# Kernel optimization log

Hardware: AMD Instinct MI355X
Metric: run time of the kernel (lower is better)

The kernel has to match this reference:

```python
import jax, jax.numpy as jnp
import numpy as np

B, N = 2, 256
RC = 6.0
BOX = 12.0
# (center_radius, eta) for G2; kappas for G3; (eta, zeta, lambda) for G4/G5
G2_PARAMS = [(rs, eta) for rs in (0.0, 2.0) for eta in (0.1, 1.0)]
G3_KAPPAS = [1.0, 2.0]
G45_PARAMS = [(eta, zeta, lam) for eta in (0.01, 0.1) for zeta in (1.0, 4.0) for lam in (-1.0, 1.0)]


def _fc(r, rc):
    # Behler cosine cutoff: 0.5*(cos(pi r / rc) + 1) for r < rc, else 0
    return 0.5 * (jnp.cos(jnp.pi * r / rc) + 1.0) * (r < rc)


def setup_inputs() -> dict:
    key = jax.random.key(0)
    k1, k2 = jax.random.split(key)
    atomic_numbers = jax.random.randint(k1, (N,), 1, 10).astype(jnp.float32)
    coordinates = jax.random.uniform(k2, (B, N, 3), dtype=jnp.float32) * BOX
    return {"atomic_numbers": atomic_numbers, "coordinates": coordinates}


def reference(atomic_numbers, coordinates):
    b, n, _ = coordinates.shape
    # r_ij vector = x_i - x_j, matching coords.unsqueeze(-2) - coords.unsqueeze(-3)
    dvec = coordinates[:, :, None, :] - coordinates[:, None, :, :]        # [B,N,N,3]
    sq = jnp.sum(dvec * dvec, axis=-1)                                    # [B,N,N]
    pair_mask = ~jnp.eye(n, dtype=bool)                                   # j != i
    sq_safe = jnp.where(pair_mask, sq, 1.0)
    r = jnp.where(pair_mask, jnp.sqrt(sq_safe), 0.0)                      # [B,N,N]
    fcr = _fc(r, RC) * pair_mask                                          # cutoff, self excluded

    feats = [jnp.broadcast_to(atomic_numbers, (b, n))]
    # G1: sum_j fc(r_ij)
    feats.append(jnp.sum(fcr, axis=-1))
    # G2: sum_j exp(-eta*(r_ij - Rs)^2) * fc(r_ij)
    for rs, eta in G2_PARAMS:
        feats.append(jnp.sum(jnp.exp(-eta * (r - rs) ** 2) * fcr, axis=-1))
    # G3: sum_j cos(kappa * r_ij) * fc(r_ij)
    for kappa in G3_KAPPAS:
        feats.append(jnp.sum(jnp.cos(kappa * r) * fcr, axis=-1))

    # shared angular (triplet) quantities, each [B,N,N,N]
    dot = jnp.einsum('bijc,bikc->bijk', dvec, dvec)
    denom = r[:, :, :, None] * r[:, :, None, :]
    cos_t = dot / jnp.where(denom > 0, denom, 1.0)
    sq_ij = sq[:, :, :, None]
    sq_ik = sq[:, :, None, :]
    sq_jk = sq[:, None, :, :]
    sq3 = sq_ij + sq_ik + sq_jk
    sq2 = sq_ij + sq_ik
    # fc products: fcr already zero on the diagonal, so fc3 vanishes whenever
    # j==i, k==i, or j==k (full triplet mask for G4)
    fc3 = fcr[:, :, :, None] * fcr[:, :, None, :] * fcr[:, None, :, :]
    fc2 = fcr[:, :, :, None] * fcr[:, :, None, :] * pair_mask[None, None, :, :]

    # G4: 2^(1-zeta) sum_{j!=k} (1+lam*cos)^zeta exp(-eta*(rij^2+rik^2+rjk^2)) fc fc fc
    for eta, zeta, lam in G45_PARAMS:
        ang = jnp.maximum(1.0 + lam * cos_t, 0.0) ** zeta
        feats.append((2.0 ** (1.0 - zeta)) * jnp.sum(ang * jnp.exp(-eta * sq3) * fc3, axis=(-2, -1)))
    # G5: 2^(1-zeta) sum_{j!=k} (1+lam*cos)^zeta exp(-eta*(rij^2+rik^2)) fc fc
    for eta, zeta, lam in G45_PARAMS:
        ang = jnp.maximum(1.0 + lam * cos_t, 0.0) ** zeta
        feats.append((2.0 ** (1.0 - zeta)) * jnp.sum(ang * jnp.exp(-eta * sq2) * fc2, axis=(-2, -1)))

    return jnp.stack(feats, axis=-1)  # [B, N, 24]
```

## Files before the change

### kernel.cpp

```cpp
#include <hip/hip_runtime.h>
#include <math.h>

#define NN 256
#define NF 24
#define RCUT 6.0f
#define PI_F 3.14159265358979323846f
#define NSEG 8

__global__ __launch_bounds__(512, 4) void feat_kernel(
    const float* __restrict__ Z,
    const float* __restrict__ coords,
    float* __restrict__ out)
{
    const int i = blockIdx.x, b = blockIdx.y;
    const int tid = threadIdx.x, lane = tid & 63, wave = tid >> 6;

    __shared__ float4 geo[NN];
    __shared__ float2 ab[NN];
    __shared__ int   wave_cnt[4];
    __shared__ float rad[4][7];
    __shared__ float red2[8][8][16];

    const float* cb = coords + (size_t)b * NN * 3;
    const float xi = cb[i * 3 + 0], yi = cb[i * 3 + 1], zi = cb[i * 3 + 2];

    float dx = 0, dy = 0, dz = 0, r2 = 0, r = 0, fc = 0;
    bool incut = false;
    if (tid < NN) {
        const float xj = cb[tid * 3 + 0], yj = cb[tid * 3 + 1], zj = cb[tid * 3 + 2];
        dx = xi - xj; dy = yi - yj; dz = zi - zj;
        r2 = dx * dx + dy * dy + dz * dz;
        r  = sqrtf(r2);
        incut = (tid != i) && (r < RCUT);
        fc = incut ? 0.5f * (__cosf((PI_F / RCUT) * r) + 1.0f) : 0.0f;

        float racc[7];
        racc[0] = fc;
        racc[1] = __expf(-0.1f * r2) * fc;
        racc[2] = __expf(-1.0f * r2) * fc;
        const float d = r - 2.0f;
        racc[3] = __expf(-0.1f * d * d) * fc;
        racc[4] = __expf(-1.0f * d * d) * fc;
        racc[5] = __cosf(r) * fc;
        racc[6] = __cosf(2.0f * r) * fc;
#pragma unroll
        for (int t = 0; t < 7; t++) {
            float v = racc[t];
            for (int off = 32; off > 0; off >>= 1) v += __shfl_down(v, off, 64);
            if (lane == 0) rad[wave][t] = v;
        }
        const unsigned long long bal = __ballot(incut);
        if (lane == 0) wave_cnt[wave] = __popcll(bal);
    }
    __syncthreads();

    const int m = wave_cnt[0] + wave_cnt[1] + wave_cnt[2] + wave_cnt[3];
    if (tid < NN && incut) {
        const unsigned long long bal = __ballot(incut);
        int base = 0;
#pragma unroll
        for (int w = 0; w < 4; w++) if (w < wave) base += wave_cnt[w];
        const int p = base + __popcll(bal & ((1ULL << lane) - 1ULL));
        geo[p] = make_float4(dx, dy, dz, 1.0f / r);
        ab[p]  = make_float2(fc * __expf(-0.01f * r2), fc * __expf(-0.1f * r2));
    }
    __syncthreads();

    float acc[16];
#pragma unroll
    for (int t = 0; t < 16; t++) acc[t] = 0.0f;

    if (m >= 2) {
        const int Rfull = (m - 1) >> 1;
        const int tlo = 1 + (Rfull * wave) / NSEG;
        const int thi = (Rfull * (wave + 1)) / NSEG;
        const bool halfseg = (wave == NSEG - 1) && ((m & 1) == 0);
        const int mh = m >> 1;
        for (int rnd = 0; rnd < 4; ++rnd) {
            const int jj = lane + (rnd << 6);
            if (jj >= m) break;
            const float4 gj = geo[jj];
            const float2 aj = ab[jj];
            const int tend = thi + ((halfseg && jj < mh) ? 1 : 0);
#pragma unroll 2
            for (int t = tlo; t <= tend; ++t) {
                int kk = jj + ((t > thi) ? mh : t); if (kk >= m) kk -= m;
                const float4 g = geo[kk];
                const float2 a = ab[kk];
                const float ddx = gj.x - g.x, ddy = gj.y - g.y, ddz = gj.z - g.z;
                const float sqjk = ddx * ddx + ddy * ddy + ddz * ddz;
                const float rjk = sqrtf(sqjk);
                const float fcjk = (rjk < RCUT) ? 0.5f * (__cosf((PI_F / RCUT) * rjk) + 1.0f) : 0.0f;
                const float dot = gj.x * g.x + gj.y * g.y + gj.z * g.z;
                const float cost = dot * gj.w * g.w;
                const float w2a = aj.x * a.x;
                const float w2b = aj.y * a.y;
                const float t3a = fcjk * __expf(-0.01f * sqjk);
                const float t3b = fcjk * __expf(-0.1f * sqjk);
                const float w3a = w2a * t3a, w3b = w2b * t3b;
                const float c1m = 1.0f - cost;
                const float c1p = 1.0f + cost;
                const float c2m = c1m * c1m, c2p = c1p * c1p;
                const float c4m = c2m * c2m, c4p = c2p * c2p;
                acc[0]  += c1m * w3a;  acc[1]  += c1p * w3a;
                acc[2]  += c4m * w3a;  acc[3]  += c4p * w3a;
                acc[4]  += c1m * w3b;  acc[5]  += c1p * w3b;
                acc[6]  += c4m * w3b;  acc[7]  += c4p * w3b;
                acc[8]  += c1m * w2a;  acc[9]  += c1p * w2a;
                acc[10] += c4m * w2a;  acc[11] += c4p * w2a;
                acc[12] += c1m * w2b;  acc[13] += c1p * w2b;
                acc[14] += c4m * w2b;  acc[15] += c4p * w2b;
            }
        }
    }

#pragma unroll
    for (int t = 0; t < 16; t++) {
        float v = acc[t];
        v += __shfl_down(v, 32, 64);
        v += __shfl_down(v, 16, 64);
        v += __shfl_down(v, 8, 64);
        acc[t] = v;
    }
    if (lane < 8) {
#pragma unroll
        for (int t = 0; t < 16; t++) red2[wave][lane][t] = acc[t];
    }
    __syncthreads();

    float* ob = out + ((size_t)b * NN + i) * NF;
    if (tid < 128) {
        const int f = tid >> 3, s = tid & 7;
        float v = 0.0f;
#pragma unroll
        for (int w = 0; w < 8; w++) v += red2[w][s][f];
        v += __shfl_down(v, 4, 8);
        v += __shfl_down(v, 2, 8);
        v += __shfl_down(v, 1, 8);
        if (s == 0) {
            v *= ((f & 3) >= 2) ? 0.25f : 2.0f;
            ob[8 + f] = v;
        }
    } else if (tid >= 128 && tid < 135) {
        const int t = tid - 128;
        ob[1 + t] = rad[0][t] + rad[1][t] + rad[2][t] + rad[3][t];
    } else if (tid == 135) {
        ob[0] = Z[i];
    }
}

extern "C" void kernel_launch(void* const* d_in, const int* in_sizes, int n_in,
                              void* d_out, int out_size, void* d_ws, size_t ws_size,
                              hipStream_t stream) {
    const float* Z = (const float*)d_in[0];
    const float* coords = (const float*)d_in[1];
    float* out = (float*)d_out;
    feat_kernel<<<dim3(NN, 2), dim3(512), 0, stream>>>(Z, coords, out);
}
```

Baseline: 65.86 us.

## Split G4 and G5 triplet sums across separate blocks, replicate neighbor list

Launches a third grid dimension so that one block per atom computes the G4 (three-cutoff) accumulators and another computes the G5 (two-cutoff) ones, halving per-thread accumulators. The neighbor arrays are extended with a wrapped copy so the inner loop indexes kk = jj + t directly, with no modulo branch. The G5 half skips the sqrt, cos and exp work on r_jk. In exchange the neighbor-list construction is duplicated across both blocks, the block count doubles, and the two halves carry unequal work.

Result: no change. 65.52 us (-0.5%).

```diff
diff --git a/kernel.cpp b/kernel.cpp
--- a/kernel.cpp
+++ b/kernel.cpp
@@ -7,19 +7,84 @@
 #define PI_F 3.14159265358979323846f
 #define NSEG 8
 
+template <bool TRIPLE>
+__device__ __forceinline__ void pair_loop(
+    const float4* __restrict__ geo, const float2* __restrict__ ab,
+    int m, int wave, int lane, float* acc)
+{
+    const int Rfull = (m - 1) >> 1;
+    const int tlo = 1 + ((Rfull * wave) >> 3);
+    const int thi = (Rfull * (wave + 1)) >> 3;
+    const int mh = m >> 1;
+    for (int rnd = 0; rnd < 4; ++rnd) {
+        const int jj = lane + (rnd << 6);
+        if (jj >= m) break;
+        const float4 gj = geo[jj];
+        const float2 aj = ab[jj];
+        for (int t = tlo; t <= thi; ++t) {
+            const int kk = jj + t;
+            const float4 g = geo[kk];
+            const float2 a = ab[kk];
+            const float dot = gj.x * g.x + gj.y * g.y + gj.z * g.z;
+            const float cost = dot * gj.w * g.w;
+            float wa = aj.x * a.x;
+            float wb = aj.y * a.y;
+            if (TRIPLE) {
+                const float ddx = gj.x - g.x, ddy = gj.y - g.y, ddz = gj.z - g.z;
+                const float sqjk = ddx * ddx + ddy * ddy + ddz * ddz;
+                const float rjk = sqrtf(sqjk);
+                const float fcjk = (rjk < RCUT) ? 0.5f * (__cosf((PI_F / RCUT) * rjk) + 1.0f) : 0.0f;
+                wa *= fcjk * __expf(-0.01f * sqjk);
+                wb *= fcjk * __expf(-0.1f * sqjk);
+            }
+            const float c1m = 1.0f - cost, c1p = 1.0f + cost;
+            const float c2m = c1m * c1m, c2p = c1p * c1p;
+            const float c4m = c2m * c2m, c4p = c2p * c2p;
+            acc[0] += c1m * wa;  acc[1] += c1p * wa;
+            acc[2] += c4m * wa;  acc[3] += c4p * wa;
+            acc[4] += c1m * wb;  acc[5] += c1p * wb;
+            acc[6] += c4m * wb;  acc[7] += c4p * wb;
+        }
+        if (wave == NSEG - 1 && (m & 1) == 0 && jj < mh) {
+            const int kk = jj + mh;
+            const float4 g = geo[kk];
+            const float2 a = ab[kk];
+            const float dot = gj.x * g.x + gj.y * g.y + gj.z * g.z;
+            const float cost = dot * gj.w * g.w;
+            float wa = aj.x * a.x;
+            float wb = aj.y * a.y;
+            if (TRIPLE) {
+                const float ddx = gj.x - g.x, ddy = gj.y - g.y, ddz = gj.z - g.z;
+                const float sqjk = ddx * ddx + ddy * ddy + ddz * ddz;
+                const float rjk = sqrtf(sqjk);
+                const float fcjk = (rjk < RCUT) ? 0.5f * (__cosf((PI_F / RCUT) * rjk) + 1.0f) : 0.0f;
+                wa *= fcjk * __expf(-0.01f * sqjk);
+                wb *= fcjk * __expf(-0.1f * sqjk);
+            }
+            const float c1m = 1.0f - cost, c1p = 1.0f + cost;
+            const float c2m = c1m * c1m, c2p = c1p * c1p;
+            const float c4m = c2m * c2m, c4p = c2p * c2p;
+            acc[0] += c1m * wa;  acc[1] += c1p * wa;
+            acc[2] += c4m * wa;  acc[3] += c4p * wa;
+            acc[4] += c1m * wb;  acc[5] += c1p * wb;
+            acc[6] += c4m * wb;  acc[7] += c4p * wb;
+        }
+    }
+}
+
 __global__ __launch_bounds__(512, 4) void feat_kernel(
     const float* __restrict__ Z,
     const float* __restrict__ coords,
     float* __restrict__ out)
 {
-    const int i = blockIdx.x, b = blockIdx.y;
+    const int i = blockIdx.x, b = blockIdx.y, half = blockIdx.z;
     const int tid = threadIdx.x, lane = tid & 63, wave = tid >> 6;
 
-    __shared__ float4 geo[NN];
-    __shared__ float2 ab[NN];
+    __shared__ float4 geo[NN + 128];
+    __shared__ float2 ab[NN + 128];
     __shared__ int   wave_cnt[4];
     __shared__ float rad[4][7];
-    __shared__ float red2[8][8][16];
+    __shared__ float red2[8][8][8];
 
     const float* cb = coords + (size_t)b * NN * 3;
     const float xi = cb[i * 3 + 0], yi = cb[i * 3 + 1], zi = cb[i * 3 + 2];
@@ -33,21 +98,22 @@
         r  = sqrtf(r2);
         incut = (tid != i) && (r < RCUT);
         fc = incut ? 0.5f * (__cosf((PI_F / RCUT) * r) + 1.0f) : 0.0f;
-
-        float racc[7];
-        racc[0] = fc;
-        racc[1] = __expf(-0.1f * r2) * fc;
-        racc[2] = __expf(-1.0f * r2) * fc;
-        const float d = r - 2.0f;
-        racc[3] = __expf(-0.1f * d * d) * fc;
-        racc[4] = __expf(-1.0f * d * d) * fc;
-        racc[5] = __cosf(r) * fc;
-        racc[6] = __cosf(2.0f * r) * fc;
+        if (half == 0) {
+            float racc[7];
+            racc[0] = fc;
+            racc[1] = __expf(-0.1f * r2) * fc;
+            racc[2] = __expf(-1.0f * r2) * fc;
+            const float d = r - 2.0f;
+            racc[3] = __expf(-0.1f * d * d) * fc;
+            racc[4] = __expf(-1.0f * d * d) * fc;
+            racc[5] = __cosf(r) * fc;
+            racc[6] = __cosf(2.0f * r) * fc;
 #pragma unroll
-        for (int t = 0; t < 7; t++) {
-            float v = racc[t];
-            for (int off = 32; off > 0; off >>= 1) v += __shfl_down(v, off, 64);
-            if (lane == 0) rad[wave][t] = v;
+            for (int t = 0; t < 7; t++) {
+                float v = racc[t];
+                for (int off = 32; off > 0; off >>= 1) v += __shfl_down(v, off, 64);
+                if (lane == 0) rad[wave][t] = v;
+            }
         }
         const unsigned long long bal = __ballot(incut);
         if (lane == 0) wave_cnt[wave] = __popcll(bal);
@@ -65,57 +131,20 @@
         ab[p]  = make_float2(fc * __expf(-0.01f * r2), fc * __expf(-0.1f * r2));
     }
     __syncthreads();
+    const int Rext = (m >= 2) ? ((m - 1) >> 1) : 0;
+    for (int s = tid; s < Rext; s += 512) { geo[m + s] = geo[s]; ab[m + s] = ab[s]; }
+    __syncthreads();
 
-    float acc[16];
+    float acc[8];
 #pragma unroll
-    for (int t = 0; t < 16; t++) acc[t] = 0.0f;
-
+    for (int t = 0; t < 8; t++) acc[t] = 0.0f;
     if (m >= 2) {
-        const int Rfull = (m - 1) >> 1;
-        const int tlo = 1 + (Rfull * wave) / NSEG;
-        const int thi = (Rfull * (wave + 1)) / NSEG;
-        const bool halfseg = (wave == NSEG - 1) && ((m & 1) == 0);
-        const int mh = m >> 1;
-        for (int rnd = 0; rnd < 4; ++rnd) {
-            const int jj = lane + (rnd << 6);
-            if (jj >= m) break;
-            const float4 gj = geo[jj];
-            const float2 aj = ab[jj];
-            const int tend = thi + ((halfseg && jj < mh) ? 1 : 0);
-#pragma unroll 2
-            for (int t = tlo; t <= tend; ++t) {
-                int kk = jj + ((t > thi) ? mh : t); if (kk >= m) kk -= m;
-                const float4 g = geo[kk];
-                const float2 a = ab[kk];
-                const float ddx = gj.x - g.x, ddy = gj.y - g.y, ddz = gj.z - g.z;
-                const float sqjk = ddx * ddx + ddy * ddy + ddz * ddz;
-                const float rjk = sqrtf(sqjk);
-                const float fcjk = (rjk < RCUT) ? 0.5f * (__cosf((PI_F / RCUT) * rjk) + 1.0f) : 0.0f;
-                const float dot = gj.x * g.x + gj.y * g.y + gj.z * g.z;
-                const float cost = dot * gj.w * g.w;
-                const float w2a = aj.x * a.x;
-                const float w2b = aj.y * a.y;
-                const float t3a = fcjk * __expf(-0.01f * sqjk);
-                const float t3b = fcjk * __expf(-0.1f * sqjk);
-                const float w3a = w2a * t3a, w3b = w2b * t3b;
-                const float c1m = 1.0f - cost;
-                const float c1p = 1.0f + cost;
-                const float c2m = c1m * c1m, c2p = c1p * c1p;
-                const float c4m = c2m * c2m, c4p = c2p * c2p;
-                acc[0]  += c1m * w3a;  acc[1]  += c1p * w3a;
-                acc[2]  += c4m * w3a;  acc[3]  += c4p * w3a;
-                acc[4]  += c1m * w3b;  acc[5]  += c1p * w3b;
-                acc[6]  += c4m * w3b;  acc[7]  += c4p * w3b;
-                acc[8]  += c1m * w2a;  acc[9]  += c1p * w2a;
-                acc[10] += c4m * w2a;  acc[11] += c4p * w2a;
-                acc[12] += c1m * w2b;  acc[13] += c1p * w2b;
-                acc[14] += c4m * w2b;  acc[15] += c4p * w2b;
-            }
-        }
+        if (half == 0) pair_loop<true>(geo, ab, m, wave, lane, acc);
+        else           pair_loop<false>(geo, ab, m, wave, lane, acc);
     }
 
 #pragma unroll
-    for (int t = 0; t < 16; t++) {
+    for (int t = 0; t < 8; t++) {
         float v = acc[t];
         v += __shfl_down(v, 32, 64);
         v += __shfl_down(v, 16, 64);
@@ -124,12 +153,12 @@
     }
     if (lane < 8) {
 #pragma unroll
-        for (int t = 0; t < 16; t++) red2[wave][lane][t] = acc[t];
+        for (int t = 0; t < 8; t++) red2[wave][lane][t] = acc[t];
     }
     __syncthreads();
 
     float* ob = out + ((size_t)b * NN + i) * NF;
-    if (tid < 128) {
+    if (tid < 64) {
         const int f = tid >> 3, s = tid & 7;
         float v = 0.0f;
 #pragma unroll
@@ -139,12 +168,12 @@
         v += __shfl_down(v, 1, 8);
         if (s == 0) {
             v *= ((f & 3) >= 2) ? 0.25f : 2.0f;
-            ob[8 + f] = v;
+            ob[(half ? 16 : 8) + f] = v;
         }
-    } else if (tid >= 128 && tid < 135) {
-        const int t = tid - 128;
+    } else if (half == 0 && tid >= 64 && tid < 71) {
+        const int t = tid - 64;
         ob[1 + t] = rad[0][t] + rad[1][t] + rad[2][t] + rad[3][t];
-    } else if (tid == 135) {
+    } else if (half == 0 && tid == 71) {
         ob[0] = Z[i];
     }
 }
@@ -155,5 +184,5 @@
     const float* Z = (const float*)d_in[0];
     const float* coords = (const float*)d_in[1];
     float* out = (float*)d_out;
-    feat_kernel<<<dim3(NN, 2), dim3(512), 0, stream>>>(Z, coords, out);
+    feat_kernel<<<dim3(NN, 2, 2), dim3(512), 0, stream>>>(Z, coords, out);
 }
```

## Compute G5 via angular moment tensors and use polynomial cutoff for G4

Applied to the files above, without the earlier changes.

G5 has no j-k cutoff, so the kernel now computes it in closed form from weighted moment sums of unit vectors up to fourth order (the (1±cos)^zeta expansion). Two waves accumulate these moments in O(m) work while six waves run the pairwise G4 triplet loop, which drops from 16 to 8 accumulators. In that loop, r_jk^2 is derived from the stored r_ij and r_ik and the cosine (law of cosines), and the cosine cutoff becomes a Taylor polynomial in r_jk^2, removing the sqrt and cos. Shared arrays are extended with wrapped copies to avoid the modulo. The risks are float cancellation in the moment expansion and approximation error in the polynomial.

Result: faster. 63.81 us (-3.1%).

```diff
diff --git a/kernel.cpp b/kernel.cpp
--- a/kernel.cpp
+++ b/kernel.cpp
@@ -5,7 +5,18 @@
 #define NF 24
 #define RCUT 6.0f
 #define PI_F 3.14159265358979323846f
-#define NSEG 8
+#define CS 0.27415568f
+
+__device__ __forceinline__ float fc_poly(float u) {
+    float p = 1.0438378e-9f;
+    p = fmaf(p, u, -1.3778659e-7f);
+    p = fmaf(p, u,  1.2400794e-5f);
+    p = fmaf(p, u, -6.9444444e-4f);
+    p = fmaf(p, u,  2.0833333e-2f);
+    p = fmaf(p, u, -0.25f);
+    p = fmaf(p, u,  1.0f);
+    return p;
+}
 
 __global__ __launch_bounds__(512, 4) void feat_kernel(
     const float* __restrict__ Z,
@@ -15,11 +26,13 @@
     const int i = blockIdx.x, b = blockIdx.y;
     const int tid = threadIdx.x, lane = tid & 63, wave = tid >> 6;
 
-    __shared__ float4 geo[NN];
-    __shared__ float2 ab[NN];
+    __shared__ float4 geo[NN + 128];
+    __shared__ float4 ab[NN + 128];
     __shared__ int   wave_cnt[4];
     __shared__ float rad[4][7];
-    __shared__ float red2[8][8][16];
+    __shared__ float red[6][8][8];
+    __shared__ float mom[2][64][36];
+    __shared__ float momsum[2][36];
 
     const float* cb = coords + (size_t)b * NN * 3;
     const float xi = cb[i * 3 + 0], yi = cb[i * 3 + 1], zi = cb[i * 3 + 2];
@@ -33,7 +46,6 @@
         r  = sqrtf(r2);
         incut = (tid != i) && (r < RCUT);
         fc = incut ? 0.5f * (__cosf((PI_F / RCUT) * r) + 1.0f) : 0.0f;
-
         float racc[7];
         racc[0] = fc;
         racc[1] = __expf(-0.1f * r2) * fc;
@@ -61,79 +73,119 @@
 #pragma unroll
         for (int w = 0; w < 4; w++) if (w < wave) base += wave_cnt[w];
         const int p = base + __popcll(bal & ((1ULL << lane) - 1ULL));
-        geo[p] = make_float4(dx, dy, dz, 1.0f / r);
-        ab[p]  = make_float2(fc * __expf(-0.01f * r2), fc * __expf(-0.1f * r2));
-    }
-    __syncthreads();
-
-    float acc[16];
-#pragma unroll
-    for (int t = 0; t < 16; t++) acc[t] = 0.0f;
-
-    if (m >= 2) {
-        const int Rfull = (m - 1) >> 1;
-        const int tlo = 1 + (Rfull * wave) / NSEG;
-        const int thi = (Rfull * (wave + 1)) / NSEG;
-        const bool halfseg = (wave == NSEG - 1) && ((m & 1) == 0);
-        const int mh = m >> 1;
+        const float rinv = 1.0f / r;
+        geo[p] = make_float4(dx * rinv, dy * rinv, dz * rinv, r);
+        ab[p]  = make_float4(fc * __expf(-0.01f * r2), fc * __expf(-0.1f * r2), r2, 0.0f);
+    }
+    __syncthreads();
+    const int Rext = (m >= 2) ? ((m - 1) >> 1) : 0;
+    for (int s = tid; s < Rext; s += 512) { geo[m + s] = geo[s]; ab[m + s] = ab[s]; }
+    __syncthreads();
+
+    if (wave < 6) {
+        float acc[8];
+#pragma unroll
+        for (int t = 0; t < 8; t++) acc[t] = 0.0f;
+        if (m >= 2) {
+            const int Rfull = (m - 1) >> 1;
+            const int tlo = 1 + (Rfull * wave) / 6;
+            const int thi = (Rfull * (wave + 1)) / 6;
+            const int mh = m >> 1;
+            const bool doHalf = (wave == 5) && ((m & 1) == 0);
+            for (int rnd = 0; rnd < 4; ++rnd) {
+                const int jj = lane + (rnd << 6);
+                if (jj >= m) break;
+                const float4 gj = geo[jj];
+                const float4 aj = ab[jj];
+                const float r2j = aj.z;
+                const float gw2 = -2.0f * gj.w;
+                const int tend = thi + ((doHalf && jj < mh) ? 1 : 0);
+                for (int t = tlo; t <= tend; ++t) {
+                    const int kk = jj + ((t > thi) ? mh : t);
+                    const float4 g = geo[kk];
+                    const float4 a = ab[kk];
+                    const float cost = fmaf(gj.x, g.x, fmaf(gj.y, g.y, gj.z * g.z));
+                    const float s = fmaf(gw2 * g.w, cost, r2j + a.z);
+                    const float pfc = fc_poly(CS * s);
+                    const float fcjk = (s < 36.0f) ? pfc : 0.0f;
+                    const float ea = __expf(-0.01f * s);
+                    const float eb = __expf(-0.1f * s);
+                    const float wa = (aj.x * a.x) * (fcjk * ea);
+                    const float wb = (aj.y * a.y) * (fcjk * eb);
+                    const float c1m = 1.0f - cost, c1p = 1.0f + cost;
+                    const float c2m = c1m * c1m, c2p = c1p * c1p;
+                    const float c4m = c2m * c2m, c4p = c2p * c2p;
+                    acc[0] += c1m * wa;  acc[1] += c1p * wa;
+                    acc[2] += c4m * wa;  acc[3] += c4p * wa;
+                    acc[4] += c1m * wb;  acc[5] += c1p * wb;
+                    acc[6] += c4m * wb;  acc[7] += c4p * wb;
+                }
+            }
+        }
+#pragma unroll
+        for (int t = 0; t < 8; t++) {
+            float v = acc[t];
+            v += __shfl_down(v, 32, 64);
+            v += __shfl_down(v, 16, 64);
+            v += __shfl_down(v, 8, 64);
+            acc[t] = v;
+        }
+        if (lane < 8) {
+#pragma unroll
+            for (int t = 0; t < 8; t++) red[wave][lane][t] = acc[t];
+        }
+    } else {
+        const int e = wave - 6;
+        float mm[36];
+#pragma unroll
+        for (int q = 0; q < 36; q++) mm[q] = 0.0f;
         for (int rnd = 0; rnd < 4; ++rnd) {
             const int jj = lane + (rnd << 6);
             if (jj >= m) break;
-            const float4 gj = geo[jj];
-            const float2 aj = ab[jj];
-            const int tend = thi + ((halfseg && jj < mh) ? 1 : 0);
-#pragma unroll 2
-            for (int t = tlo; t <= tend; ++t) {
-                int kk = jj + ((t > thi) ? mh : t); if (kk >= m) kk -= m;
-                const float4 g = geo[kk];
-                const float2 a = ab[kk];
-                const float ddx = gj.x - g.x, ddy = gj.y - g.y, ddz = gj.z - g.z;
-                const float sqjk = ddx * ddx + ddy * ddy + ddz * ddz;
-                const float rjk = sqrtf(sqjk);
-                const float fcjk = (rjk < RCUT) ? 0.5f * (__cosf((PI_F / RCUT) * rjk) + 1.0f) : 0.0f;
-                const float dot = gj.x * g.x + gj.y * g.y + gj.z * g.z;
-                const float cost = dot * gj.w * g.w;
-                const float w2a = aj.x * a.x;
-                const float w2b = aj.y * a.y;
-                const float t3a = fcjk * __expf(-0.01f * sqjk);
-                const float t3b = fcjk * __expf(-0.1f * sqjk);
-                const float w3a = w2a * t3a, w3b = w2b * t3b;
-                const float c1m = 1.0f - cost;
-                const float c1p = 1.0f + cost;
-                const float c2m = c1m * c1m, c2p = c1p * c1p;
-                const float c4m = c2m * c2m, c4p = c2p * c2p;
-                acc[0]  += c1m * w3a;  acc[1]  += c1p * w3a;
-                acc[2]  += c4m * w3a;  acc[3]  += c4p * w3a;
-                acc[4]  += c1m * w3b;  acc[5]  += c1p * w3b;
-                acc[6]  += c4m * w3b;  acc[7]  += c4p * w3b;
-                acc[8]  += c1m * w2a;  acc[9]  += c1p * w2a;
-                acc[10] += c4m * w2a;  acc[11] += c4p * w2a;
-                acc[12] += c1m * w2b;  acc[13] += c1p * w2b;
-                acc[14] += c4m * w2b;  acc[15] += c4p * w2b;
+            const float4 g = geo[jj];
+            const float4 a = ab[jj];
+            const float w = (e == 0) ? a.x : a.y;
+            const float x = g.x, y = g.y, z = g.z;
+            mm[0] += w;
+            const float wx = w * x, wy = w * y, wz = w * z;
+            mm[1] += wx; mm[2] += wy; mm[3] += wz;
+            const float wxx = wx * x, wxy = wx * y, wxz = wx * z;
+            const float wyy = wy * y, wyz = wy * z, wzz = wz * z;
+            mm[4] += wxx; mm[5] += wxy; mm[6] += wxz;
+            mm[7] += wyy; mm[8] += wyz; mm[9] += wzz;
+            const float wxxx = wxx * x, wxxy = wxx * y, wxxz = wxx * z;
+            const float wxyy = wxy * y, wxyz = wxy * z, wxzz = wxz * z;
+            const float wyyy = wyy * y, wyyz = wyy * z, wyzz = wyz * z, wzzz = wzz * z;
+            mm[10] += wxxx; mm[11] += wxxy; mm[12] += wxxz; mm[13] += wxyy;
+            mm[14] += wxyz; mm[15] += wxzz; mm[16] += wyyy; mm[17] += wyyz;
+            mm[18] += wyzz; mm[19] += wzzz;
+            mm[20] += wxxx * x; mm[21] += wxxx * y; mm[22] += wxxx * z;
+            mm[23] += wxxy * y; mm[24] += wxxy * z; mm[25] += wxxz * z;
+            mm[26] += wxyy * y; mm[27] += wxyy * z; mm[28] += wxyz * z;
+            mm[29] += wxzz * z; mm[30] += wyyy * y; mm[31] += wyyy * z;
+            mm[32] += wyyz * z; mm[33] += wyzz * z; mm[34] += wzzz * z;
+            mm[35] = fmaf(w, w, mm[35]);
+        }
+#pragma unroll
+        for (int q = 0; q < 36; q++) mom[e][lane][q] = mm[q];
+        if (lane < 36) {
+            float v0 = 0, v1 = 0, v2 = 0, v3 = 0;
+#pragma unroll
+            for (int j = 0; j < 64; j += 4) {
+                v0 += mom[e][j + 0][lane]; v1 += mom[e][j + 1][lane];
+                v2 += mom[e][j + 2][lane]; v3 += mom[e][j + 3][lane];
             }
-        }
-    }
-
-#pragma unroll
-    for (int t = 0; t < 16; t++) {
-        float v = acc[t];
-        v += __shfl_down(v, 32, 64);
-        v += __shfl_down(v, 16, 64);
-        v += __shfl_down(v, 8, 64);
-        acc[t] = v;
-    }
-    if (lane < 8) {
-#pragma unroll
-        for (int t = 0; t < 16; t++) red2[wave][lane][t] = acc[t];
+            momsum[e][lane] = (v0 + v1) + (v2 + v3);
+        }
     }
     __syncthreads();
 
     float* ob = out + ((size_t)b * NN + i) * NF;
-    if (tid < 128) {
+    if (tid < 64) {
         const int f = tid >> 3, s = tid & 7;
         float v = 0.0f;
 #pragma unroll
-        for (int w = 0; w < 8; w++) v += red2[w][s][f];
+        for (int w = 0; w < 6; w++) v += red[w][s][f];
         v += __shfl_down(v, 4, 8);
         v += __shfl_down(v, 2, 8);
         v += __shfl_down(v, 1, 8);
@@ -141,10 +193,33 @@
             v *= ((f & 3) >= 2) ? 0.25f : 2.0f;
             ob[8 + f] = v;
         }
-    } else if (tid >= 128 && tid < 135) {
-        const int t = tid - 128;
+    } else if (tid < 72) {
+        const int f = tid - 64, e = f >> 2, sub = f & 3;
+        const float* M = momsum[e];
+        const float S0 = M[0] * M[0];
+        const float S1 = M[1] * M[1] + M[2] * M[2] + M[3] * M[3];
+        const float S2 = M[4] * M[4] + M[7] * M[7] + M[9] * M[9]
+                       + 2.f * (M[5] * M[5] + M[6] * M[6] + M[8] * M[8]);
+        const float S3 = M[10] * M[10] + M[16] * M[16] + M[19] * M[19]
+                       + 3.f * (M[11] * M[11] + M[12] * M[12] + M[13] * M[13]
+                              + M[15] * M[15] + M[17] * M[17] + M[18] * M[18])
+                       + 6.f * M[14] * M[14];
+        const float S4 = M[20] * M[20] + M[30] * M[30] + M[34] * M[34]
+                       + 4.f * (M[21] * M[21] + M[22] * M[22] + M[26] * M[26]
+                              + M[29] * M[29] + M[31] * M[31] + M[33] * M[33])
+                       + 6.f * (M[23] * M[23] + M[25] * M[25] + M[32] * M[32])
+                       + 12.f * (M[24] * M[24] + M[27] * M[27] + M[28] * M[28]);
+        const float D = M[35];
+        const float lam = (sub & 1) ? 1.0f : -1.0f;
+        float v;
+        if (sub < 2) v = S0 + lam * S1 - (1.0f + lam) * D;
+        else         v = 0.125f * (S0 + 6.f * S2 + S4 + lam * 4.f * (S1 + S3)
+                                   - ((sub == 3) ? 16.f * D : 0.0f));
+        ob[16 + f] = v;
+    } else if (tid < 79) {
+        const int t = tid - 72;
         ob[1 + t] = rad[0][t] + rad[1][t] + rad[2][t] + rad[3][t];
-    } else if (tid == 135) {
+    } else if (tid == 79) {
         ob[0] = Z[i];
     }
 }
```
